# Kernel optimization log

Hardware: AMD Instinct MI355X
Metric: run time of the kernel (lower is better)

## Reference

```python
import jax, jax.numpy as jnp
import numpy as np

N, E, R, H = 50000, 800000, 8, 1  # nodes, edges, relations, heads
IN_DIM = HID = OUT = 128
NEG_SLOPE = 0.2  # PyG RGATConv default


def _rgat_layer(x, W, q, k, b, src, dst, etype):
    """One RGATConv (additive-self-attention, across-relation softmax, dim=1).
    x: [N, Cin]; W: [R, Cin, H*C]; q,k: [H*C, H]; b: [H*C]."""
    n = x.shape[0]
    xr = jnp.einsum('nc,rcd->rnd', x, W)            # [R, N, H*C] per-relation transform
    qproj = jnp.einsum('rnd,dh->rnh', xr, q)        # [R, N, H]
    kproj = jnp.einsum('rnd,dh->rnh', xr, k)        # [R, N, H]
    out_j = xr[etype, src]                          # [E, H*C] transformed source feats
    alpha = jax.nn.leaky_relu(qproj[etype, dst] + kproj[etype, src], NEG_SLOPE)  # [E, H]
    # per-destination-node softmax over incoming edges (across relations)
    amax = jax.ops.segment_max(alpha, dst, num_segments=n)
    amax = jnp.where(jnp.isfinite(amax), amax, 0.0)
    ex = jnp.exp(alpha - amax[dst])                 # [E, H]
    denom = jax.ops.segment_sum(ex, dst, num_segments=n)
    alpha = ex / (denom[dst] + 1e-16)
    d = out_j.shape[1]
    c = d // H
    msg = (alpha[:, :, None] * out_j.reshape(-1, H, c)).reshape(-1, d)  # [E, H*C]
    out = jax.ops.segment_sum(msg, dst, num_segments=n)                  # [N, H*C]
    return out + b


def setup_inputs() -> dict:
    key = jax.random.key(0)
    ks = jax.random.split(key, 16)
    inp = {
        'x': jax.random.normal(ks[0], (N, IN_DIM), dtype=jnp.float32),
        'edge_index': jax.random.randint(ks[1], (2, E), 0, N, dtype=jnp.int32),
        'edge_type': jax.random.randint(ks[2], (E,), 0, R, dtype=jnp.int32),
    }
    dims = [(IN_DIM, HID), (HID, HID), (HID, OUT)]
    for i, (cin, cout) in enumerate(dims):
        d = H * cout
        s = 1.0 / np.sqrt(cin)
        inp[f'W{i}'] = jax.random.normal(ks[3 + 4 * i], (R, cin, d), dtype=jnp.float32) * s
        inp[f'q{i}'] = jax.random.normal(ks[4 + 4 * i], (d, H), dtype=jnp.float32) * (1.0 / np.sqrt(d))
        inp[f'k{i}'] = jax.random.normal(ks[5 + 4 * i], (d, H), dtype=jnp.float32) * (1.0 / np.sqrt(d))
        inp[f'b{i}'] = jnp.zeros((d,), dtype=jnp.float32)
    return inp


def reference(x, edge_index, edge_type, W0, q0, k0, b0, W1, q1, k1, b1, W2, q2, k2, b2):
    src, dst = edge_index[0], edge_index[1]
    h = jax.nn.relu(_rgat_layer(x, W0, q0, k0, b0, src, dst, edge_type))
    h = jax.nn.relu(_rgat_layer(h, W1, q1, k1, b1, src, dst, edge_type))
    return _rgat_layer(h, W2, q2, k2, b2, src, dst, edge_type)
```

## Files before the change

kernel.cpp:

```cpp
#include <hip/hip_runtime.h>
#include <hip/hip_bf16.h>
#include <cstdint>
#include <cstddef>

#define NNODES 50000
#define NEDGES 800000
#define NREL 8
#define DIM 128
#define NOUT 1024
#define NEG_SLOPE 0.2f
#define NFRAG 16640

typedef __attribute__((ext_vector_type(8))) short short8;
typedef __attribute__((ext_vector_type(4))) float f32x4;

static __device__ __forceinline__ short f2bf(float v) {
  union { float f; unsigned u; } c; c.f = v;
  unsigned u = c.u;
  unsigned r = (u + 0x7fffu + ((u >> 16) & 1u)) >> 16;
  return (short)r;
}
static __device__ __forceinline__ float bf2f(short s) {
  union { unsigned u; float f; } c; c.u = ((unsigned)(unsigned short)s) << 16;
  return c.f;
}


__global__ void k_hist(const int* __restrict__ ei, const int* __restrict__ et,
                       int* __restrict__ cnt, int E) {
  int e = blockIdx.x * 256 + threadIdx.x;
  if (e < E) {
    int d = ei[E + e];
    int t = et[e];
    atomicAdd(&cnt[d * NREL + t], 1);
  }
}

__global__ void k_scan_reduce(const int* __restrict__ cnt, int* __restrict__ sums, int n) {
  __shared__ int sd[256];
  int base = blockIdx.x * 4096;
  int t = threadIdx.x;
  int acc = 0;
  for (int i = t; i < 4096; i += 256) {
    int idx = base + i;
    if (idx < n) acc += cnt[idx];
  }
  sd[t] = acc; __syncthreads();
  for (int s = 128; s > 0; s >>= 1) {
    if (t < s) sd[t] += sd[t + s];
    __syncthreads();
  }
  if (t == 0) sums[blockIdx.x] = sd[0];
}

__global__ void k_scan_top(int* sums, int nb) {
  __shared__ int sd[128];
  int t = threadIdx.x;
  int v = (t < nb) ? sums[t] : 0;
  sd[t] = v; __syncthreads();
  for (int s = 1; s < 128; s <<= 1) {
    int u = (t >= s) ? sd[t - s] : 0;
    __syncthreads();
    sd[t] += u;
    __syncthreads();
  }
  if (t < nb) sums[t] = sd[t] - v;
}

__global__ void k_scan_final(const int* __restrict__ cnt, const int* __restrict__ sums,
                             int* __restrict__ offs, int* __restrict__ cur,
                             int n, int E) {
  __shared__ int sd[256];
  int base = blockIdx.x * 4096;
  int t = threadIdx.x;
  int run = sums[blockIdx.x];
  for (int c = 0; c < 16; c++) {
    int idx = base + c * 256 + t;
    int v = (idx < n) ? cnt[idx] : 0;
    sd[t] = v; __syncthreads();
    for (int s = 1; s < 256; s <<= 1) {
      int u = (t >= s) ? sd[t - s] : 0;
      __syncthreads();
      sd[t] += u;
      __syncthreads();
    }
    if (idx < n) {
      int e0 = run + sd[t] - v;
      offs[idx] = e0;
      cur[idx] = e0;
    }
    run += sd[255];
    __syncthreads();
  }
  if (blockIdx.x == 0 && t == 0) offs[n] = E;
}

__global__ void k_scatter(const int* __restrict__ ei, const int* __restrict__ et,
                          int* __restrict__ cursor, int* __restrict__ pk, int E) {
  int e = blockIdx.x * 256 + threadIdx.x;
  if (e < E) {
    int s = ei[e];
    int d = ei[E + e];
    int t = et[e];
    int pos = atomicAdd(&cursor[d * NREL + t], 1);
    pk[pos] = s | (t << 16);
  }
}


__global__ void k_wprep(const float* __restrict__ W, const float* __restrict__ q,
                        const float* __restrict__ kk, short* __restrict__ Wfh,
                        short* __restrict__ Wfl) {
  int b = blockIdx.x;
  if (b < 64) {
    int id = b * 256 + threadIdx.x;
    int l = id & 63;
    int kc = (id >> 6) & 3;
    int n16 = id >> 8;
    int n = n16 * 16 + (l & 15);
    int r = n >> 7, nn = n & 127;
    int k0 = kc * 32 + (l >> 4) * 8;
    short8 vh, vl;
#pragma unroll
    for (int j = 0; j < 8; j++) {
      float v = W[((size_t)r * DIM + k0 + j) * DIM + nn];
      short h = f2bf(v);
      vh[j] = h;
      vl[j] = f2bf(v - bf2f(h));
    }
    ((short8*)Wfh)[id] = vh;
    ((short8*)Wfl)[id] = vl;
  } else {
    int tid = threadIdx.x;
    int kc = tid >> 6, l = tid & 63;
    int np = l & 15;
    int k0 = kc * 32 + (l >> 4) * 8;
    const float* vec = (np < 8) ? q : kk;
    const float* wbase = W + ((size_t)(np & 7) * DIM) * DIM;
    short8 vh, vl;
#pragma unroll
    for (int j = 0; j < 8; j++) {
      const float* wrow = wbase + (size_t)(k0 + j) * DIM;
      float acc = 0.f;
#pragma unroll 8
      for (int d = 0; d < DIM; d++) acc += wrow[d] * vec[d];
      short h = f2bf(acc);
      vh[j] = h;
      vl[j] = f2bf(acc - bf2f(h));
    }
    int fid = (256 + kc) * 64 + l;
    ((short8*)Wfh)[fid] = vh;
    ((short8*)Wfl)[fid] = vl;
  }
}

#define APITCH 272

__global__ __launch_bounds__(256, 3) void k_xr(
    const float* __restrict__ A, const short* __restrict__ Wfh,
    const short* __restrict__ Wfl, float* __restrict__ xr,
    float* __restrict__ qp, float* __restrict__ kp, int M, int nmt) {
  __shared__ char sAh[64 * APITCH];
  __shared__ char sAl[64 * APITCH];
  int lin = blockIdx.x;
  int nwg8 = (nmt * 4) >> 3;
  int g = (lin & 7) * nwg8 + (lin >> 3);
  int mt0 = g >> 2, nb = g & 3;
  int m0 = mt0 * 64;
  int t = threadIdx.x, w = t >> 6, l = t & 63;

  {
    int row = t >> 2, q4 = t & 3;
    int m = m0 + row;
    const float4* src = (const float4*)(A + (size_t)m * DIM + q4 * 32);
    float4 z = make_float4(0.f, 0.f, 0.f, 0.f);
#pragma unroll
    for (int u = 0; u < 4; u++) {
      float4 va = (m < M) ? src[2 * u] : z;
      float4 vb = (m < M) ? src[2 * u + 1] : z;
      float vv[8] = {va.x, va.y, va.z, va.w, vb.x, vb.y, vb.z, vb.w};
      short8 hh, ll;
#pragma unroll
      for (int j = 0; j < 8; j++) {
        short h = f2bf(vv[j]);
        hh[j] = h;
        ll[j] = f2bf(vv[j] - bf2f(h));
      }
      int off = row * APITCH + (q4 * 4 + u) * 16;
      *(short8*)(sAh + off) = hh;
      *(short8*)(sAl + off) = ll;
    }
  }
  __syncthreads();

  f32x4 acc[4][4];
  f32x4 accqk[4];
  f32x4 zero = {0.f, 0.f, 0.f, 0.f};
#pragma unroll
  for (int mt = 0; mt < 4; mt++) {
#pragma unroll
    for (int nt = 0; nt < 4; nt++) acc[mt][nt] = zero;
    accqk[mt] = zero;
  }

  int r16 = l & 15, hi16 = l >> 4;
  int n16base = nb * 16 + w * 4;
  int doqk = (w == 0 && nb == 0);
#pragma unroll
  for (int kc = 0; kc < 4; kc++) {
    short8 fsh[4], fsl[4];
#pragma unroll
    for (int mt = 0; mt < 4; mt++) {
      int row = mt * 16 + r16;
      int off = row * APITCH + (kc * 4 + hi16) * 16;
      fsh[mt] = *(const short8*)(sAh + off);
      fsl[mt] = *(const short8*)(sAl + off);
    }
#pragma unroll
    for (int nt = 0; nt < 4; nt++) {
      size_t fid = ((size_t)(n16base + nt) * 4 + kc) * 64 + l;
      short8 ah = ((const short8*)Wfh)[fid];
      short8 al = ((const short8*)Wfl)[fid];
#pragma unroll
      for (int mt = 0; mt < 4; mt++) {
        acc[mt][nt] = __builtin_amdgcn_mfma_f32_16x16x32_bf16(ah, fsh[mt], acc[mt][nt], 0, 0, 0);
        acc[mt][nt] = __builtin_amdgcn_mfma_f32_16x16x32_bf16(ah, fsl[mt], acc[mt][nt], 0, 0, 0);
        acc[mt][nt] = __builtin_amdgcn_mfma_f32_16x16x32_bf16(al, fsh[mt], acc[mt][nt], 0, 0, 0);
      }
    }
    if (doqk) {
      size_t fid = (size_t)(256 + kc) * 64 + l;
      short8 bh = ((const short8*)Wfh)[fid];
      short8 bl = ((const short8*)Wfl)[fid];
#pragma unroll
      for (int mt = 0; mt < 4; mt++) {
        accqk[mt] = __builtin_amdgcn_mfma_f32_16x16x32_bf16(bh, fsh[mt], accqk[mt], 0, 0, 0);
        accqk[mt] = __builtin_amdgcn_mfma_f32_16x16x32_bf16(bh, fsl[mt], accqk[mt], 0, 0, 0);
        accqk[mt] = __builtin_amdgcn_mfma_f32_16x16x32_bf16(bl, fsh[mt], accqk[mt], 0, 0, 0);
      }
    }
  }
#pragma unroll
  for (int mt = 0; mt < 4; mt++) {
    int m = m0 + mt * 16 + r16;
    if (m >= M) continue;
#pragma unroll
    for (int nt = 0; nt < 4; nt++) {
      int n = nb * 256 + w * 64 + nt * 16 + hi16 * 4;
      f32x4 a = acc[mt][nt];
      float4 o; o.x = a.x; o.y = a.y; o.z = a.z; o.w = a.w;
      *(float4*)(xr + (size_t)m * NOUT + n) = o;
    }
    if (doqk) {
      float* dst = (hi16 < 2) ? (qp + (size_t)m * NREL + (hi16 & 1) * 4)
                              : (kp + (size_t)m * NREL + (hi16 & 1) * 4);
      f32x4 a = accqk[mt];
      float4 o; o.x = a.x; o.y = a.y; o.z = a.z; o.w = a.w;
      *(float4*)dst = o;
    }
  }
}

__global__ void k_agg_out(const float* __restrict__ xr, const float* __restrict__ qp,
                          const float* __restrict__ kp, const int* __restrict__ offs,
                          const int* __restrict__ pk, const float* __restrict__ bias,
                          float* __restrict__ out, int N, int relu) {
  int wid = (blockIdx.x * blockDim.x + threadIdx.x) >> 6;
  int lane = threadIdx.x & 63;
  if (wid >= N) return;
  int base = wid * NREL;
  int start = offs[base], end = offs[base + NREL];
  float a0 = 0.f, a1 = 0.f;
  if (start < end) {
    float m = -1e30f, s = 0.f;
    for (int i = start + lane; i < end; i += 64) {
      int p = pk[i];
      int src = p & 0xffff, tt = p >> 16;
      float a = qp[base + tt] + kp[src * NREL + tt];
      a = (a > 0.f) ? a : NEG_SLOPE * a;
      float mn = fmaxf(m, a);
      s = s * __expf(m - mn) + __expf(a - mn);
      m = mn;
    }
    for (int d = 32; d > 0; d >>= 1) {
      float mo = __shfl_xor(m, d);
      float so = __shfl_xor(s, d);
      float mn = fmaxf(m, mo);
      s = s * __expf(m - mn) + so * __expf(mo - mn);
      m = mn;
    }
    float inv = 1.f / (s + 1e-16f);
    int i = start;
    for (; i + 4 <= end; i += 4) {
      int p0 = pk[i], p1 = pk[i + 1], p2 = pk[i + 2], p3 = pk[i + 3];
      float2 xv0 = ((const float2*)(xr + (((size_t)(p0 & 0xffff)) * NREL + (p0 >> 16)) * DIM))[lane];
      float2 xv1 = ((const float2*)(xr + (((size_t)(p1 & 0xffff)) * NREL + (p1 >> 16)) * DIM))[lane];
      float2 xv2 = ((const float2*)(xr + (((size_t)(p2 & 0xffff)) * NREL + (p2 >> 16)) * DIM))[lane];
      float2 xv3 = ((const float2*)(xr + (((size_t)(p3 & 0xffff)) * NREL + (p3 >> 16)) * DIM))[lane];
      float aa0 = qp[base + (p0 >> 16)] + kp[(p0 & 0xffff) * NREL + (p0 >> 16)];
      float aa1 = qp[base + (p1 >> 16)] + kp[(p1 & 0xffff) * NREL + (p1 >> 16)];
      float aa2 = qp[base + (p2 >> 16)] + kp[(p2 & 0xffff) * NREL + (p2 >> 16)];
      float aa3 = qp[base + (p3 >> 16)] + kp[(p3 & 0xffff) * NREL + (p3 >> 16)];
      aa0 = (aa0 > 0.f) ? aa0 : NEG_SLOPE * aa0;
      aa1 = (aa1 > 0.f) ? aa1 : NEG_SLOPE * aa1;
      aa2 = (aa2 > 0.f) ? aa2 : NEG_SLOPE * aa2;
      aa3 = (aa3 > 0.f) ? aa3 : NEG_SLOPE * aa3;
      float w0 = __expf(aa0 - m) * inv;
      float w1 = __expf(aa1 - m) * inv;
      float w2 = __expf(aa2 - m) * inv;
      float w3 = __expf(aa3 - m) * inv;
      a0 = fmaf(w0, xv0.x, a0); a1 = fmaf(w0, xv0.y, a1);
      a0 = fmaf(w1, xv1.x, a0); a1 = fmaf(w1, xv1.y, a1);
      a0 = fmaf(w2, xv2.x, a0); a1 = fmaf(w2, xv2.y, a1);
      a0 = fmaf(w3, xv3.x, a0); a1 = fmaf(w3, xv3.y, a1);
    }
    for (; i < end; i++) {
      int p = pk[i];
      int src = p & 0xffff, tt = p >> 16;
      float2 xv = ((const float2*)(xr + ((size_t)src * NREL + tt) * DIM))[lane];
      float a = qp[base + tt] + kp[src * NREL + tt];
      a = (a > 0.f) ? a : NEG_SLOPE * a;
      float wg = __expf(a - m) * inv;
      a0 = fmaf(wg, xv.x, a0);
      a1 = fmaf(wg, xv.y, a1);
    }
  }
  float2 bv = ((const float2*)bias)[lane];
  a0 += bv.x; a1 += bv.y;
  if (relu) { a0 = fmaxf(a0, 0.f); a1 = fmaxf(a1, 0.f); }
  float2 o; o.x = a0; o.y = a1;
  ((float2*)(out + (size_t)wid * DIM))[lane] = o;
}


extern "C" void kernel_launch(void* const* d_in, const int* in_sizes, int n_in,
                              void* d_out, int out_size, void* d_ws, size_t ws_size,
                              hipStream_t stream) {
  const float* x = (const float*)d_in[0];
  const int* ei = (const int*)d_in[1];
  const int* et = (const int*)d_in[2];
  const float* Wl3[3] = {(const float*)d_in[3], (const float*)d_in[7], (const float*)d_in[11]};
  const float* ql[3] = {(const float*)d_in[4], (const float*)d_in[8], (const float*)d_in[12]};
  const float* kl[3] = {(const float*)d_in[5], (const float*)d_in[9], (const float*)d_in[13]};
  const float* bl[3] = {(const float*)d_in[6], (const float*)d_in[10], (const float*)d_in[14]};
  float* out = (float*)d_out;

  char* w = (char*)d_ws;
  auto alloc = [&](size_t bytes) -> char* {
    char* p = w;
    w += (bytes + 255) & ~(size_t)255;
    return p;
  };
  const int NK = NNODES * NREL;
  float* xr = (float*)alloc((size_t)NNODES * NOUT * 4);
  int* cnt = (int*)alloc((size_t)NK * 4);
  int* offs = (int*)alloc((size_t)(NK + 1) * 4);
  int* cursor = (int*)alloc((size_t)NK * 4);
  int* sums = (int*)alloc(256 * 4);
  int* pk = (int*)alloc((size_t)NEDGES * 4);
  float* qp = (float*)alloc((size_t)NNODES * NREL * 4);
  float* kp = (float*)alloc((size_t)NNODES * NREL * 4);
  short* Wfh = (short*)alloc((size_t)NFRAG * 16);
  short* Wfl = (short*)alloc((size_t)NFRAG * 16);
  float* h1 = (float*)alloc((size_t)NNODES * DIM * 4);
  float* h2 = (float*)alloc((size_t)NNODES * DIM * 4);

  hipMemsetAsync(cnt, 0, (size_t)NK * 4, stream);
  k_hist<<<(NEDGES + 255) / 256, 256, 0, stream>>>(ei, et, cnt, NEDGES);
  int nchunk = (NK + 4095) / 4096;
  k_scan_reduce<<<nchunk, 256, 0, stream>>>(cnt, sums, NK);
  k_scan_top<<<1, 128, 0, stream>>>(sums, nchunk);
  k_scan_final<<<nchunk, 256, 0, stream>>>(cnt, sums, offs, cursor, NK, NEDGES);
  k_scatter<<<(NEDGES + 255) / 256, 256, 0, stream>>>(ei, et, cursor, pk, NEDGES);

  const float* hin = x;
  float* houts[3] = {h1, h2, out};
  const int nmt = (NNODES + 63) / 64;
  for (int l = 0; l < 3; l++) {
    k_wprep<<<65, 256, 0, stream>>>(Wl3[l], ql[l], kl[l], Wfh, Wfl);
    k_xr<<<nmt * 4, 256, 0, stream>>>(hin, Wfh, Wfl, xr, qp, kp, NNODES, nmt);
    k_agg_out<<<(NNODES + 3) / 4, 256, 0, stream>>>(xr, qp, kp, offs, pk, bl[l],
                                                    houts[l], NNODES, l < 2 ? 1 : 0);
    hin = houts[l];
  }
}
```

Before: 835.2 us.

## Double-buffer two row tiles per xr block and drop softmax max pass

```diff
diff --git a/kernel.cpp b/kernel.cpp
--- a/kernel.cpp
+++ b/kernel.cpp
@@ -156,28 +156,36 @@
 
 #define APITCH 272
 
-__global__ __launch_bounds__(256, 3) void k_xr(
+__global__ __launch_bounds__(256, 2) void k_xr(
     const float* __restrict__ A, const short* __restrict__ Wfh,
     const short* __restrict__ Wfl, float* __restrict__ xr,
-    float* __restrict__ qp, float* __restrict__ kp, int M, int nmt) {
-  __shared__ char sAh[64 * APITCH];
-  __shared__ char sAl[64 * APITCH];
+    float* __restrict__ qp, float* __restrict__ kp, int M, int npair) {
+  __shared__ char sAh[2][64 * APITCH];
+  __shared__ char sAl[2][64 * APITCH];
   int lin = blockIdx.x;
-  int nwg8 = (nmt * 4) >> 3;
-  int g = (lin & 7) * nwg8 + (lin >> 3);
-  int mt0 = g >> 2, nb = g & 3;
-  int m0 = mt0 * 64;
+  int nwg = npair * 4;
+  int q8 = nwg >> 3, r8 = nwg & 7;
+  int xcd = lin & 7, pos = lin >> 3;
+  int g = (xcd < r8 ? xcd * (q8 + 1) : r8 * (q8 + 1) + (xcd - r8) * q8) + pos;
+  int mpair = g >> 2, nb = g & 3;
+  int m0 = mpair * 128;
   int t = threadIdx.x, w = t >> 6, l = t & 63;
-
-  {
-    int row = t >> 2, q4 = t & 3;
-    int m = m0 + row;
+  int row = t >> 2, q4 = t & 3;
+  int r16 = l & 15, hi16 = l >> 4;
+  int n16base = nb * 16 + w * 4;
+  int doqk = (w == 0 && nb == 0);
+
+  auto loadA = [&](float4* ra, int mbase) {
+    int m = mbase + row;
     const float4* src = (const float4*)(A + (size_t)m * DIM + q4 * 32);
     float4 z = make_float4(0.f, 0.f, 0.f, 0.f);
 #pragma unroll
+    for (int u = 0; u < 8; u++) ra[u] = (m < M) ? src[u] : z;
+  };
+  auto stageW = [&](int buf, const float4* ra) {
+#pragma unroll
     for (int u = 0; u < 4; u++) {
-      float4 va = (m < M) ? src[2 * u] : z;
-      float4 vb = (m < M) ? src[2 * u + 1] : z;
+      float4 va = ra[2 * u], vb = ra[2 * u + 1];
       float vv[8] = {va.x, va.y, va.z, va.w, vb.x, vb.y, vb.z, vb.w};
       short8 hh, ll;
 #pragma unroll
@@ -187,78 +195,84 @@
         ll[j] = f2bf(vv[j] - bf2f(h));
       }
       int off = row * APITCH + (q4 * 4 + u) * 16;
-      *(short8*)(sAh + off) = hh;
-      *(short8*)(sAl + off) = ll;
-    }
-  }
+      *(short8*)(sAh[buf] + off) = hh;
+      *(short8*)(sAl[buf] + off) = ll;
+    }
+  };
+  auto computeT = [&](int buf, int mbase) {
+    f32x4 acc[4][4];
+    f32x4 accqk[4];
+    f32x4 zero = {0.f, 0.f, 0.f, 0.f};
+#pragma unroll
+    for (int mt = 0; mt < 4; mt++) {
+#pragma unroll
+      for (int nt = 0; nt < 4; nt++) acc[mt][nt] = zero;
+      accqk[mt] = zero;
+    }
+#pragma unroll
+    for (int kc = 0; kc < 4; kc++) {
+      short8 fsh[4], fsl[4];
+#pragma unroll
+      for (int mt = 0; mt < 4; mt++) {
+        int rr = mt * 16 + r16;
+        int off = rr * APITCH + (kc * 4 + hi16) * 16;
+        fsh[mt] = *(const short8*)(sAh[buf] + off);
+        fsl[mt] = *(const short8*)(sAl[buf] + off);
+      }
+#pragma unroll
+      for (int nt = 0; nt < 4; nt++) {
+        size_t fid = ((size_t)(n16base + nt) * 4 + kc) * 64 + l;
+        short8 ah = ((const short8*)Wfh)[fid];
+        short8 al = ((const short8*)Wfl)[fid];
+#pragma unroll
+        for (int mt = 0; mt < 4; mt++) {
+          acc[mt][nt] = __builtin_amdgcn_mfma_f32_16x16x32_bf16(ah, fsh[mt], acc[mt][nt], 0, 0, 0);
+          acc[mt][nt] = __builtin_amdgcn_mfma_f32_16x16x32_bf16(ah, fsl[mt], acc[mt][nt], 0, 0, 0);
+          acc[mt][nt] = __builtin_amdgcn_mfma_f32_16x16x32_bf16(al, fsh[mt], acc[mt][nt], 0, 0, 0);
+        }
+      }
+      if (doqk) {
+        size_t fid = (size_t)(256 + kc) * 64 + l;
+        short8 bh = ((const short8*)Wfh)[fid];
+        short8 bl = ((const short8*)Wfl)[fid];
+#pragma unroll
+        for (int mt = 0; mt < 4; mt++) {
+          accqk[mt] = __builtin_amdgcn_mfma_f32_16x16x32_bf16(bh, fsh[mt], accqk[mt], 0, 0, 0);
+          accqk[mt] = __builtin_amdgcn_mfma_f32_16x16x32_bf16(bh, fsl[mt], accqk[mt], 0, 0, 0);
+          accqk[mt] = __builtin_amdgcn_mfma_f32_16x16x32_bf16(bl, fsh[mt], accqk[mt], 0, 0, 0);
+        }
+      }
+    }
+#pragma unroll
+    for (int mt = 0; mt < 4; mt++) {
+      int m = mbase + mt * 16 + r16;
+      if (m >= M) continue;
+#pragma unroll
+      for (int nt = 0; nt < 4; nt++) {
+        int n = nb * 256 + w * 64 + nt * 16 + hi16 * 4;
+        f32x4 a = acc[mt][nt];
+        float4 o; o.x = a.x; o.y = a.y; o.z = a.z; o.w = a.w;
+        *(float4*)(xr + (size_t)m * NOUT + n) = o;
+      }
+      if (doqk) {
+        float* dst = (hi16 < 2) ? (qp + (size_t)m * NREL + (hi16 & 1) * 4)
+                                : (kp + (size_t)m * NREL + (hi16 & 1) * 4);
+        f32x4 a = accqk[mt];
+        float4 o; o.x = a.x; o.y = a.y; o.z = a.z; o.w = a.w;
+        *(float4*)dst = o;
+      }
+    }
+  };
+
+  float4 ra[8];
+  loadA(ra, m0);
+  stageW(0, ra);
   __syncthreads();
-
-  f32x4 acc[4][4];
-  f32x4 accqk[4];
-  f32x4 zero = {0.f, 0.f, 0.f, 0.f};
-#pragma unroll
-  for (int mt = 0; mt < 4; mt++) {
-#pragma unroll
-    for (int nt = 0; nt < 4; nt++) acc[mt][nt] = zero;
-    accqk[mt] = zero;
-  }
-
-  int r16 = l & 15, hi16 = l >> 4;
-  int n16base = nb * 16 + w * 4;
-  int doqk = (w == 0 && nb == 0);
-#pragma unroll
-  for (int kc = 0; kc < 4; kc++) {
-    short8 fsh[4], fsl[4];
-#pragma unroll
-    for (int mt = 0; mt < 4; mt++) {
-      int row = mt * 16 + r16;
-      int off = row * APITCH + (kc * 4 + hi16) * 16;
-      fsh[mt] = *(const short8*)(sAh + off);
-      fsl[mt] = *(const short8*)(sAl + off);
-    }
-#pragma unroll
-    for (int nt = 0; nt < 4; nt++) {
-      size_t fid = ((size_t)(n16base + nt) * 4 + kc) * 64 + l;
-      short8 ah = ((const short8*)Wfh)[fid];
-      short8 al = ((const short8*)Wfl)[fid];
-#pragma unroll
-      for (int mt = 0; mt < 4; mt++) {
-        acc[mt][nt] = __builtin_amdgcn_mfma_f32_16x16x32_bf16(ah, fsh[mt], acc[mt][nt], 0, 0, 0);
-        acc[mt][nt] = __builtin_amdgcn_mfma_f32_16x16x32_bf16(ah, fsl[mt], acc[mt][nt], 0, 0, 0);
-        acc[mt][nt] = __builtin_amdgcn_mfma_f32_16x16x32_bf16(al, fsh[mt], acc[mt][nt], 0, 0, 0);
-      }
-    }
-    if (doqk) {
-      size_t fid = (size_t)(256 + kc) * 64 + l;
-      short8 bh = ((const short8*)Wfh)[fid];
-      short8 bl = ((const short8*)Wfl)[fid];
-#pragma unroll
-      for (int mt = 0; mt < 4; mt++) {
-        accqk[mt] = __builtin_amdgcn_mfma_f32_16x16x32_bf16(bh, fsh[mt], accqk[mt], 0, 0, 0);
-        accqk[mt] = __builtin_amdgcn_mfma_f32_16x16x32_bf16(bh, fsl[mt], accqk[mt], 0, 0, 0);
-        accqk[mt] = __builtin_amdgcn_mfma_f32_16x16x32_bf16(bl, fsh[mt], accqk[mt], 0, 0, 0);
-      }
-    }
-  }
-#pragma unroll
-  for (int mt = 0; mt < 4; mt++) {
-    int m = m0 + mt * 16 + r16;
-    if (m >= M) continue;
-#pragma unroll
-    for (int nt = 0; nt < 4; nt++) {
-      int n = nb * 256 + w * 64 + nt * 16 + hi16 * 4;
-      f32x4 a = acc[mt][nt];
-      float4 o; o.x = a.x; o.y = a.y; o.z = a.z; o.w = a.w;
-      *(float4*)(xr + (size_t)m * NOUT + n) = o;
-    }
-    if (doqk) {
-      float* dst = (hi16 < 2) ? (qp + (size_t)m * NREL + (hi16 & 1) * 4)
-                              : (kp + (size_t)m * NREL + (hi16 & 1) * 4);
-      f32x4 a = accqk[mt];
-      float4 o; o.x = a.x; o.y = a.y; o.z = a.z; o.w = a.w;
-      *(float4*)dst = o;
-    }
-  }
+  loadA(ra, m0 + 64);
+  computeT(0, m0);
+  stageW(1, ra);
+  __syncthreads();
+  computeT(1, m0 + 64);
 }
 
 __global__ void k_agg_out(const float* __restrict__ xr, const float* __restrict__ qp,
@@ -270,63 +284,44 @@
   if (wid >= N) return;
   int base = wid * NREL;
   int start = offs[base], end = offs[base + NREL];
-  float a0 = 0.f, a1 = 0.f;
-  if (start < end) {
-    float m = -1e30f, s = 0.f;
-    for (int i = start + lane; i < end; i += 64) {
-      int p = pk[i];
-      int src = p & 0xffff, tt = p >> 16;
-      float a = qp[base + tt] + kp[src * NREL + tt];
-      a = (a > 0.f) ? a : NEG_SLOPE * a;
-      float mn = fmaxf(m, a);
-      s = s * __expf(m - mn) + __expf(a - mn);
-      m = mn;
-    }
-    for (int d = 32; d > 0; d >>= 1) {
-      float mo = __shfl_xor(m, d);
-      float so = __shfl_xor(s, d);
-      float mn = fmaxf(m, mo);
-      s = s * __expf(m - mn) + so * __expf(mo - mn);
-      m = mn;
-    }
-    float inv = 1.f / (s + 1e-16f);
-    int i = start;
-    for (; i + 4 <= end; i += 4) {
-      int p0 = pk[i], p1 = pk[i + 1], p2 = pk[i + 2], p3 = pk[i + 3];
-      float2 xv0 = ((const float2*)(xr + (((size_t)(p0 & 0xffff)) * NREL + (p0 >> 16)) * DIM))[lane];
-      float2 xv1 = ((const float2*)(xr + (((size_t)(p1 & 0xffff)) * NREL + (p1 >> 16)) * DIM))[lane];
-      float2 xv2 = ((const float2*)(xr + (((size_t)(p2 & 0xffff)) * NREL + (p2 >> 16)) * DIM))[lane];
-      float2 xv3 = ((const float2*)(xr + (((size_t)(p3 & 0xffff)) * NREL + (p3 >> 16)) * DIM))[lane];
-      float aa0 = qp[base + (p0 >> 16)] + kp[(p0 & 0xffff) * NREL + (p0 >> 16)];
-      float aa1 = qp[base + (p1 >> 16)] + kp[(p1 & 0xffff) * NREL + (p1 >> 16)];
-      float aa2 = qp[base + (p2 >> 16)] + kp[(p2 & 0xffff) * NREL + (p2 >> 16)];
-      float aa3 = qp[base + (p3 >> 16)] + kp[(p3 & 0xffff) * NREL + (p3 >> 16)];
-      aa0 = (aa0 > 0.f) ? aa0 : NEG_SLOPE * aa0;
-      aa1 = (aa1 > 0.f) ? aa1 : NEG_SLOPE * aa1;
-      aa2 = (aa2 > 0.f) ? aa2 : NEG_SLOPE * aa2;
-      aa3 = (aa3 > 0.f) ? aa3 : NEG_SLOPE * aa3;
-      float w0 = __expf(aa0 - m) * inv;
-      float w1 = __expf(aa1 - m) * inv;
-      float w2 = __expf(aa2 - m) * inv;
-      float w3 = __expf(aa3 - m) * inv;
-      a0 = fmaf(w0, xv0.x, a0); a1 = fmaf(w0, xv0.y, a1);
-      a0 = fmaf(w1, xv1.x, a0); a1 = fmaf(w1, xv1.y, a1);
-      a0 = fmaf(w2, xv2.x, a0); a1 = fmaf(w2, xv2.y, a1);
-      a0 = fmaf(w3, xv3.x, a0); a1 = fmaf(w3, xv3.y, a1);
-    }
-    for (; i < end; i++) {
-      int p = pk[i];
-      int src = p & 0xffff, tt = p >> 16;
-      float2 xv = ((const float2*)(xr + ((size_t)src * NREL + tt) * DIM))[lane];
-      float a = qp[base + tt] + kp[src * NREL + tt];
-      a = (a > 0.f) ? a : NEG_SLOPE * a;
-      float wg = __expf(a - m) * inv;
-      a0 = fmaf(wg, xv.x, a0);
-      a1 = fmaf(wg, xv.y, a1);
-    }
-  }
+  float a0 = 0.f, a1 = 0.f, ssum = 0.f;
+  int i = start;
+  for (; i + 4 <= end; i += 4) {
+    int p0 = pk[i], p1 = pk[i + 1], p2 = pk[i + 2], p3 = pk[i + 3];
+    float2 xv0 = ((const float2*)(xr + (((size_t)(p0 & 0xffff)) * NREL + (p0 >> 16)) * DIM))[lane];
+    float2 xv1 = ((const float2*)(xr + (((size_t)(p1 & 0xffff)) * NREL + (p1 >> 16)) * DIM))[lane];
+    float2 xv2 = ((const float2*)(xr + (((size_t)(p2 & 0xffff)) * NREL + (p2 >> 16)) * DIM))[lane];
+    float2 xv3 = ((const float2*)(xr + (((size_t)(p3 & 0xffff)) * NREL + (p3 >> 16)) * DIM))[lane];
+    float aa0 = qp[base + (p0 >> 16)] + kp[(p0 & 0xffff) * NREL + (p0 >> 16)];
+    float aa1 = qp[base + (p1 >> 16)] + kp[(p1 & 0xffff) * NREL + (p1 >> 16)];
+    float aa2 = qp[base + (p2 >> 16)] + kp[(p2 & 0xffff) * NREL + (p2 >> 16)];
+    float aa3 = qp[base + (p3 >> 16)] + kp[(p3 & 0xffff) * NREL + (p3 >> 16)];
+    aa0 = (aa0 > 0.f) ? aa0 : NEG_SLOPE * aa0;
+    aa1 = (aa1 > 0.f) ? aa1 : NEG_SLOPE * aa1;
+    aa2 = (aa2 > 0.f) ? aa2 : NEG_SLOPE * aa2;
+    aa3 = (aa3 > 0.f) ? aa3 : NEG_SLOPE * aa3;
+    float e0 = __expf(aa0), e1 = __expf(aa1), e2 = __expf(aa2), e3 = __expf(aa3);
+    ssum += (e0 + e1) + (e2 + e3);
+    a0 = fmaf(e0, xv0.x, a0); a1 = fmaf(e0, xv0.y, a1);
+    a0 = fmaf(e1, xv1.x, a0); a1 = fmaf(e1, xv1.y, a1);
+    a0 = fmaf(e2, xv2.x, a0); a1 = fmaf(e2, xv2.y, a1);
+    a0 = fmaf(e3, xv3.x, a0); a1 = fmaf(e3, xv3.y, a1);
+  }
+  for (; i < end; i++) {
+    int p = pk[i];
+    int src = p & 0xffff, tt = p >> 16;
+    float2 xv = ((const float2*)(xr + ((size_t)src * NREL + tt) * DIM))[lane];
+    float a = qp[base + tt] + kp[src * NREL + tt];
+    a = (a > 0.f) ? a : NEG_SLOPE * a;
+    float e = __expf(a);
+    ssum += e;
+    a0 = fmaf(e, xv.x, a0);
+    a1 = fmaf(e, xv.y, a1);
+  }
+  float inv = 1.f / (ssum + 1e-16f);
   float2 bv = ((const float2*)bias)[lane];
-  a0 += bv.x; a1 += bv.y;
+  a0 = fmaf(a0, inv, bv.x);
+  a1 = fmaf(a1, inv, bv.y);
   if (relu) { a0 = fmaxf(a0, 0.f); a1 = fmaxf(a1, 0.f); }
   float2 o; o.x = a0; o.y = a1;
   ((float2*)(out + (size_t)wid * DIM))[lane] = o;
@@ -376,9 +371,10 @@
   const float* hin = x;
   float* houts[3] = {h1, h2, out};
   const int nmt = (NNODES + 63) / 64;
+  const int npair = (nmt + 1) / 2;
   for (int l = 0; l < 3; l++) {
     k_wprep<<<65, 256, 0, stream>>>(Wl3[l], ql[l], kl[l], Wfh, Wfl);
-    k_xr<<<nmt * 4, 256, 0, stream>>>(hin, Wfh, Wfl, xr, qp, kp, NNODES, nmt);
+    k_xr<<<npair * 4, 256, 0, stream>>>(hin, Wfh, Wfl, xr, qp, kp, NNODES, npair);
     k_agg_out<<<(NNODES + 3) / 4, 256, 0, stream>>>(xr, qp, kp, offs, pk, bl[l],
                                                     houts[l], NNODES, l < 2 ? 1 : 0);
     hin = houts[l];
```

Result: slower. 904.1 us (+8.2%).

## Single-pass softmax aggregation without max subtraction, two nodes per wavefront

Applied to the files above, without the earlier changes.

```diff
diff --git a/kernel.cpp b/kernel.cpp
--- a/kernel.cpp
+++ b/kernel.cpp
@@ -156,7 +156,7 @@
 
 #define APITCH 272
 
-__global__ __launch_bounds__(256, 3) void k_xr(
+__global__ __launch_bounds__(256, 4) void k_xr(
     const float* __restrict__ A, const short* __restrict__ Wfh,
     const short* __restrict__ Wfl, float* __restrict__ xr,
     float* __restrict__ qp, float* __restrict__ kp, int M, int nmt) {
@@ -265,71 +265,55 @@
                           const float* __restrict__ kp, const int* __restrict__ offs,
                           const int* __restrict__ pk, const float* __restrict__ bias,
                           float* __restrict__ out, int N, int relu) {
-  int wid = (blockIdx.x * blockDim.x + threadIdx.x) >> 6;
+  int wv = (blockIdx.x * blockDim.x + threadIdx.x) >> 6;
   int lane = threadIdx.x & 63;
-  if (wid >= N) return;
-  int base = wid * NREL;
+  int node = wv * 2 + (lane >> 5);
+  if (node >= N) return;
+  int l32 = lane & 31;
+  int base = node * NREL;
   int start = offs[base], end = offs[base + NREL];
-  float a0 = 0.f, a1 = 0.f;
-  if (start < end) {
-    float m = -1e30f, s = 0.f;
-    for (int i = start + lane; i < end; i += 64) {
-      int p = pk[i];
-      int src = p & 0xffff, tt = p >> 16;
-      float a = qp[base + tt] + kp[src * NREL + tt];
-      a = (a > 0.f) ? a : NEG_SLOPE * a;
-      float mn = fmaxf(m, a);
-      s = s * __expf(m - mn) + __expf(a - mn);
-      m = mn;
-    }
-    for (int d = 32; d > 0; d >>= 1) {
-      float mo = __shfl_xor(m, d);
-      float so = __shfl_xor(s, d);
-      float mn = fmaxf(m, mo);
-      s = s * __expf(m - mn) + so * __expf(mo - mn);
-      m = mn;
-    }
-    float inv = 1.f / (s + 1e-16f);
-    int i = start;
-    for (; i + 4 <= end; i += 4) {
-      int p0 = pk[i], p1 = pk[i + 1], p2 = pk[i + 2], p3 = pk[i + 3];
-      float2 xv0 = ((const float2*)(xr + (((size_t)(p0 & 0xffff)) * NREL + (p0 >> 16)) * DIM))[lane];
-      float2 xv1 = ((const float2*)(xr + (((size_t)(p1 & 0xffff)) * NREL + (p1 >> 16)) * DIM))[lane];
-      float2 xv2 = ((const float2*)(xr + (((size_t)(p2 & 0xffff)) * NREL + (p2 >> 16)) * DIM))[lane];
-      float2 xv3 = ((const float2*)(xr + (((size_t)(p3 & 0xffff)) * NREL + (p3 >> 16)) * DIM))[lane];
-      float aa0 = qp[base + (p0 >> 16)] + kp[(p0 & 0xffff) * NREL + (p0 >> 16)];
-      float aa1 = qp[base + (p1 >> 16)] + kp[(p1 & 0xffff) * NREL + (p1 >> 16)];
-      float aa2 = qp[base + (p2 >> 16)] + kp[(p2 & 0xffff) * NREL + (p2 >> 16)];
-      float aa3 = qp[base + (p3 >> 16)] + kp[(p3 & 0xffff) * NREL + (p3 >> 16)];
-      aa0 = (aa0 > 0.f) ? aa0 : NEG_SLOPE * aa0;
-      aa1 = (aa1 > 0.f) ? aa1 : NEG_SLOPE * aa1;
-      aa2 = (aa2 > 0.f) ? aa2 : NEG_SLOPE * aa2;
-      aa3 = (aa3 > 0.f) ? aa3 : NEG_SLOPE * aa3;
-      float w0 = __expf(aa0 - m) * inv;
-      float w1 = __expf(aa1 - m) * inv;
-      float w2 = __expf(aa2 - m) * inv;
-      float w3 = __expf(aa3 - m) * inv;
-      a0 = fmaf(w0, xv0.x, a0); a1 = fmaf(w0, xv0.y, a1);
-      a0 = fmaf(w1, xv1.x, a0); a1 = fmaf(w1, xv1.y, a1);
-      a0 = fmaf(w2, xv2.x, a0); a1 = fmaf(w2, xv2.y, a1);
-      a0 = fmaf(w3, xv3.x, a0); a1 = fmaf(w3, xv3.y, a1);
-    }
-    for (; i < end; i++) {
-      int p = pk[i];
-      int src = p & 0xffff, tt = p >> 16;
-      float2 xv = ((const float2*)(xr + ((size_t)src * NREL + tt) * DIM))[lane];
-      float a = qp[base + tt] + kp[src * NREL + tt];
-      a = (a > 0.f) ? a : NEG_SLOPE * a;
-      float wg = __expf(a - m) * inv;
-      a0 = fmaf(wg, xv.x, a0);
-      a1 = fmaf(wg, xv.y, a1);
-    }
-  }
-  float2 bv = ((const float2*)bias)[lane];
-  a0 += bv.x; a1 += bv.y;
-  if (relu) { a0 = fmaxf(a0, 0.f); a1 = fmaxf(a1, 0.f); }
-  float2 o; o.x = a0; o.y = a1;
-  ((float2*)(out + (size_t)wid * DIM))[lane] = o;
+  float a0 = 0.f, a1 = 0.f, a2 = 0.f, a3 = 0.f, ssum = 0.f;
+  int i = start;
+  for (; i + 2 <= end; i += 2) {
+    int p0 = pk[i], p1 = pk[i + 1];
+    int s0 = p0 & 0xffff, t0 = p0 >> 16;
+    int s1 = p1 & 0xffff, t1 = p1 >> 16;
+    float4 xv0 = ((const float4*)(xr + ((size_t)s0 * NREL + t0) * DIM))[l32];
+    float4 xv1 = ((const float4*)(xr + ((size_t)s1 * NREL + t1) * DIM))[l32];
+    float aa0 = qp[base + t0] + kp[s0 * NREL + t0];
+    float aa1 = qp[base + t1] + kp[s1 * NREL + t1];
+    aa0 = (aa0 > 0.f) ? aa0 : NEG_SLOPE * aa0;
+    aa1 = (aa1 > 0.f) ? aa1 : NEG_SLOPE * aa1;
+    float e0 = __expf(aa0), e1 = __expf(aa1);
+    ssum += e0 + e1;
+    a0 = fmaf(e0, xv0.x, a0); a1 = fmaf(e0, xv0.y, a1);
+    a2 = fmaf(e0, xv0.z, a2); a3 = fmaf(e0, xv0.w, a3);
+    a0 = fmaf(e1, xv1.x, a0); a1 = fmaf(e1, xv1.y, a1);
+    a2 = fmaf(e1, xv1.z, a2); a3 = fmaf(e1, xv1.w, a3);
+  }
+  if (i < end) {
+    int p = pk[i];
+    int src = p & 0xffff, tt = p >> 16;
+    float4 xv = ((const float4*)(xr + ((size_t)src * NREL + tt) * DIM))[l32];
+    float a = qp[base + tt] + kp[src * NREL + tt];
+    a = (a > 0.f) ? a : NEG_SLOPE * a;
+    float e = __expf(a);
+    ssum += e;
+    a0 = fmaf(e, xv.x, a0); a1 = fmaf(e, xv.y, a1);
+    a2 = fmaf(e, xv.z, a2); a3 = fmaf(e, xv.w, a3);
+  }
+  float inv = 1.f / (ssum + 1e-16f);
+  float4 bv = ((const float4*)bias)[l32];
+  float4 o;
+  o.x = fmaf(a0, inv, bv.x);
+  o.y = fmaf(a1, inv, bv.y);
+  o.z = fmaf(a2, inv, bv.z);
+  o.w = fmaf(a3, inv, bv.w);
+  if (relu) {
+    o.x = fmaxf(o.x, 0.f); o.y = fmaxf(o.y, 0.f);
+    o.z = fmaxf(o.z, 0.f); o.w = fmaxf(o.w, 0.f);
+  }
+  ((float4*)(out + (size_t)node * DIM))[l32] = o;
 }
 
 
@@ -376,11 +360,12 @@
   const float* hin = x;
   float* houts[3] = {h1, h2, out};
   const int nmt = (NNODES + 63) / 64;
+  const int aggblocks = ((NNODES / 2) * 64 + 255) / 256;
   for (int l = 0; l < 3; l++) {
     k_wprep<<<65, 256, 0, stream>>>(Wl3[l], ql[l], kl[l], Wfh, Wfl);
     k_xr<<<nmt * 4, 256, 0, stream>>>(hin, Wfh, Wfl, xr, qp, kp, NNODES, nmt);
-    k_agg_out<<<(NNODES + 3) / 4, 256, 0, stream>>>(xr, qp, kp, offs, pk, bl[l],
-                                                    houts[l], NNODES, l < 2 ? 1 : 0);
+    k_agg_out<<<aggblocks, 256, 0, stream>>>(xr, qp, kp, offs, pk, bl[l],
+                                             houts[l], NNODES, l < 2 ? 1 : 0);
     hin = houts[l];
   }
 }
```

After: 961.0 us. 15.1% more time.
